# Performance work log

Measured on AMD Instinct MI355X. Metric: run time of the kernel, lower is better.

The kernel has to match this reference:

```python
import jax, jax.numpy as jnp
import numpy as np

NUM_HEADS = 12


def setup_inputs() -> dict:
    key = jax.random.key(0)
    ks = jax.random.split(key, 8)
    B, D, H, W, C = 4, 8, 14, 14, 768
    hd = C // NUM_HEADS
    return {
        "x": jax.random.normal(ks[0], (B, D, H, W, C), jnp.float32),
        "qkv_w": jax.random.normal(ks[1], (C, 3 * C), jnp.float32) * (C ** -0.5),
        "qkv_b": jax.random.normal(ks[2], (3 * C,), jnp.float32) * 0.02,
        "proj_w": jax.random.normal(ks[3], (C, C), jnp.float32) * (C ** -0.5),
        "proj_b": jax.random.normal(ks[4], (C,), jnp.float32) * 0.02,
        "rel_pos_d": jax.random.normal(ks[5], (2 * D - 1, hd), jnp.float32) * 0.02,
        "rel_pos_h": jax.random.normal(ks[6], (2 * H - 1, hd), jnp.float32) * 0.02,
        "rel_pos_w": jax.random.normal(ks[7], (2 * W - 1, hd), jnp.float32) * 0.02,
    }


def _rel_table(table, n):
    # q_size == k_size == n; relative coords in [0, 2n-2]
    idx = jnp.arange(n)[:, None] - jnp.arange(n)[None, :] + (n - 1)
    return table[idx]  # [n, n, head_dim]


def reference(x, qkv_w, qkv_b, proj_w, proj_b, rel_pos_d, rel_pos_h, rel_pos_w):
    B, D, H, W, C = x.shape
    hd = C // NUM_HEADS
    scale = hd ** -0.5
    N = D * H * W
    BH = B * NUM_HEADS

    qkv = x @ qkv_w + qkv_b  # [B,D,H,W,3C]
    qkv = qkv.reshape(B, N, 3, NUM_HEADS, hd).transpose(2, 0, 3, 1, 4).reshape(3, BH, N, hd)
    q, k, v = qkv[0], qkv[1], qkv[2]

    attn = jnp.einsum('bnc,bmc->bnm', q * scale, k)  # [BH, N, N]

    # decomposed 3D relative position bias
    Rd = _rel_table(rel_pos_d, D)  # [D,D,hd]
    Rh = _rel_table(rel_pos_h, H)  # [H,H,hd]
    Rw = _rel_table(rel_pos_w, W)  # [W,W,hd]
    r_q = q.reshape(BH, D, H, W, hd)
    rel_d = jnp.einsum('bdhwc,dkc->bdhwk', r_q, Rd)  # [BH,D,H,W,D]
    rel_h = jnp.einsum('bdhwc,hkc->bdhwk', r_q, Rh)  # [BH,D,H,W,H]
    rel_w = jnp.einsum('bdhwc,wkc->bdhwk', r_q, Rw)  # [BH,D,H,W,W]
    attn = (attn.reshape(BH, D, H, W, D, H, W)
            + rel_d[:, :, :, :, :, None, None]
            + rel_h[:, :, :, :, None, :, None]
            + rel_w[:, :, :, :, None, None, :]).reshape(BH, N, N)

    attn = jax.nn.softmax(attn, axis=-1)
    out = jnp.einsum('bnm,bmc->bnc', attn, v)  # [BH,N,hd]
    out = out.reshape(B, NUM_HEADS, D, H, W, hd).transpose(0, 2, 3, 4, 1, 5).reshape(B, D, H, W, C)
    return out @ proj_w + proj_b
```

## Files before the change

kernel.cpp:

```cpp
#include <hip/hip_runtime.h>


typedef __bf16 bf16x8 __attribute__((ext_vector_type(8)));
typedef float f32x4 __attribute__((ext_vector_type(4)));

#define MFMA16(a, b, c) __builtin_amdgcn_mfma_f32_16x16x32_bf16((a), (b), (c), 0, 0, 0)

static __device__ __forceinline__ unsigned short f2bf(float f) {
    union { float f; unsigned int u; } v; v.f = f;
    unsigned int u = v.u;
    return (unsigned short)((u + 0x7fffu + ((u >> 16) & 1u)) >> 16);
}

static __device__ __forceinline__ bf16x8 ld_bf8(const unsigned short* p) {
    return *reinterpret_cast<const bf16x8*>(p);
}

static __device__ __forceinline__ void dma16(const void* g, void* l) {
    __builtin_amdgcn_global_load_lds(
        (const __attribute__((address_space(1))) void*)g,
        (__attribute__((address_space(3))) void*)l, 16, 0, 0);
}


__global__ void k_cvt_x(const float* __restrict__ x, unsigned short* __restrict__ xbf, int n4) {
    int i = blockIdx.x * blockDim.x + threadIdx.x;
    if (i < n4) {
        float4 v = reinterpret_cast<const float4*>(x)[i];
        ushort4 o;
        o.x = f2bf(v.x); o.y = f2bf(v.y); o.z = f2bf(v.z); o.w = f2bf(v.w);
        reinterpret_cast<ushort4*>(xbf)[i] = o;
    }
}

__global__ __launch_bounds__(256) void k_transpose(const float* __restrict__ w,
                                                   unsigned short* __restrict__ wt,
                                                   int K, int N) {
    __shared__ float tile[64][65];
    int kt = blockIdx.x * 64;
    int nt = blockIdx.y * 64;
    int tid = threadIdx.x;
    int r = tid >> 2;
    int cg = tid & 3;
#pragma unroll
    for (int i = 0; i < 4; ++i) {
        int c = cg * 16 + i * 4;
        float4 v = *reinterpret_cast<const float4*>(&w[(size_t)(kt + r) * N + nt + c]);
        tile[r][c + 0] = v.x; tile[r][c + 1] = v.y; tile[r][c + 2] = v.z; tile[r][c + 3] = v.w;
    }
    __syncthreads();
#pragma unroll
    for (int i = 0; i < 4; ++i) {
        int c = cg * 16 + i * 4;
        ushort4 o;
        o.x = f2bf(tile[c + 0][r]);
        o.y = f2bf(tile[c + 1][r]);
        o.z = f2bf(tile[c + 2][r]);
        o.w = f2bf(tile[c + 3][r]);
        *reinterpret_cast<ushort4*>(&wt[(size_t)(nt + r) * K + kt + c]) = o;
    }
}

__global__ void k_tables(const float* __restrict__ rd, const float* __restrict__ rh,
                         const float* __restrict__ rw, unsigned short* __restrict__ T) {
    int i = blockIdx.x * blockDim.x + threadIdx.x;
    if (i < 80 * 64) {
        int row = i >> 6, c = i & 63;
        float v = 0.f;
        if (row < 15) v = rd[row * 64 + c];
        else if (row < 42) v = rh[(row - 15) * 64 + c];
        else if (row < 69) v = rw[(row - 42) * 64 + c];
        T[i] = f2bf(v);
    }
}

__global__ void k_fill_ind(unsigned short* __restrict__ indb) {
    int i = blockIdx.x * blockDim.x + threadIdx.x;
    if (i < 1600 * 64) {
        int key = i >> 6, c = i & 63;
        unsigned short v = 0;
        if (key < 1568) {
            int kd = key / 196;
            int r = key - kd * 196;
            int kh = r / 14;
            int kw = r - kh * 14;
            if (c == kd || c == 8 + kh || c == 22 + kw) v = 0x3F80;
        } else {
            if (c == 36) v = 0x3F80;
        }
        indb[i] = v;
    }
}

static __device__ __forceinline__ void gemm_core(const unsigned short* __restrict__ A,
                                                 const unsigned short* __restrict__ B,
                                                 int M_base, int N_base,
                                                 char* smem, f32x4 acc[4][4]) {
    const int lane = threadIdx.x & 63;
    const int wid = threadIdx.x >> 6;
    const int ww = wid & 1, wh = wid >> 1;
    const int quad = lane >> 4, l16 = lane & 15;
    const int sr = lane >> 3, sc = lane & 7;
    unsigned short* sA = (unsigned short*)smem;
    unsigned short* sB = (unsigned short*)(smem + 16384);

    for (int kt = 0; kt < 12; ++kt) {
#pragma unroll
        for (int j = 0; j < 4; ++j) {
            int loc = wid * 32 + j * 8 + sr;
            int gc = ((sc + loc) & 7) * 16;
            dma16((const char*)A + (size_t)(M_base + loc) * 1536 + kt * 128 + gc,
                  (char*)sA + (wid * 32 + j * 8) * 128);
            dma16((const char*)B + (size_t)(N_base + loc) * 1536 + kt * 128 + gc,
                  (char*)sB + (wid * 32 + j * 8) * 128);
        }
        __syncthreads();
#pragma unroll
        for (int s = 0; s < 2; ++s) {
            bf16x8 af[4], bfr[4];
#pragma unroll
            for (int i = 0; i < 4; ++i) {
                int ar = wh * 64 + i * 16 + l16;
                af[i] = ld_bf8(sA + ar * 64 + (((s * 4 + quad) - ar) & 7) * 8);
                int br = ww * 64 + i * 16 + l16;
                bfr[i] = ld_bf8(sB + br * 64 + (((s * 4 + quad) - br) & 7) * 8);
            }
#pragma unroll
            for (int i = 0; i < 4; ++i)
#pragma unroll
                for (int j2 = 0; j2 < 4; ++j2)
                    acc[i][j2] = MFMA16(af[i], bfr[j2], acc[i][j2]);
        }
        __syncthreads();
    }
}

__global__ __launch_bounds__(256, 3) void k_qkv(const unsigned short* __restrict__ xbf,
                                                const unsigned short* __restrict__ w1t,
                                                const float* __restrict__ qkv_b,
                                                unsigned short* __restrict__ qb,
                                                unsigned short* __restrict__ kb2,
                                                unsigned short* __restrict__ vb) {
    __shared__ __align__(16) char smem[32768];
    f32x4 acc[4][4] = {};
    gemm_core(xbf, w1t, blockIdx.x * 128, blockIdx.y * 128, smem, acc);

    const int lane = threadIdx.x & 63;
    const int wid = threadIdx.x >> 6;
    const int ww = wid & 1, wh = wid >> 1;
    const int quad = lane >> 4, l16 = lane & 15;
#pragma unroll
    for (int j = 0; j < 4; ++j) {
        int n = blockIdx.y * 128 + ww * 64 + j * 16 + l16;
        float bias = qkv_b[n];
        int which = n / 768;
        int rem = n - which * 768;
        int head = rem >> 6;
        int c = rem & 63;
#pragma unroll
        for (int i = 0; i < 4; ++i) {
#pragma unroll
            for (int r = 0; r < 4; ++r) {
                int m = blockIdx.x * 128 + wh * 64 + i * 16 + quad * 4 + r;
                float val = acc[i][j][r] + bias;
                int b_ = m / 1568;
                int nn = m - b_ * 1568;
                size_t idx = ((size_t)(b_ * 12 + head) * 1568 + nn) * 64 + c;
                if (which == 0)      qb[idx] = f2bf(val);
                else if (which == 1) kb2[(((size_t)(b_ * 12 + head)) * 1600 + nn) * 64 + c] = f2bf(val * 0.125f);
                else                 vb[idx] = f2bf(val);
            }
        }
    }
}

__global__ __launch_bounds__(256) void k_vt(const unsigned short* __restrict__ vb,
                                            unsigned short* __restrict__ vtb) {
    __shared__ unsigned short t[64][72];
    int bh = blockIdx.y;
    int n0 = blockIdx.x * 64;
    int tid = threadIdx.x;
    int r = tid >> 2, cg = (tid & 3) * 16;
    int n = n0 + r;
    if (n > 1567) n = 1567;
    const unsigned short* src = vb + ((size_t)bh * 1568 + n) * 64 + cg;
    *reinterpret_cast<uint4*>(&t[r][cg]) = *reinterpret_cast<const uint4*>(src);
    *reinterpret_cast<uint4*>(&t[r][cg + 8]) = *reinterpret_cast<const uint4*>(src + 8);
    __syncthreads();
    int c = tid >> 2, ng = (tid & 3) * 16;
    if (n0 + ng < 1568) {
        unsigned short buf[16];
#pragma unroll
        for (int i = 0; i < 16; ++i) buf[i] = t[ng + i][c];
        unsigned short* dst = vtb + ((size_t)bh * 64 + c) * 1600 + n0 + ng;
        *reinterpret_cast<uint4*>(dst) = *reinterpret_cast<uint4*>(&buf[0]);
        *reinterpret_cast<uint4*>(dst + 8) = *reinterpret_cast<uint4*>(&buf[8]);
    }
}

__global__ __launch_bounds__(256, 3) void k_attn(const unsigned short* __restrict__ qb,
                                                 const unsigned short* __restrict__ kb2,
                                                 const unsigned short* __restrict__ indb,
                                                 const unsigned short* __restrict__ vtb,
                                                 const unsigned short* __restrict__ Tbf,
                                                 unsigned short* __restrict__ obf) {
    __shared__ __align__(16) char smem[43008];
    unsigned short* sK = (unsigned short*)smem;
    unsigned short* sI = (unsigned short*)(smem + 8192);
    unsigned short* sV = (unsigned short*)(smem + 16384);
    const int lane = threadIdx.x & 63;
    const int wid = threadIdx.x >> 6;
    const int quad = lane >> 4;
    const int l16 = lane & 15;
    const int sr = lane >> 3;
    const int sc = lane & 7;
    const int bh = blockIdx.x;
    const int qt = blockIdx.y;

    unsigned short* pw = (unsigned short*)(smem + 24576 + wid * 4608);
    unsigned short* tR = (unsigned short*)(smem + wid * 5120);
    unsigned short* tB = (unsigned short*)(smem + 20480 + wid * 4608);

    bf16x8 a_q0[2], a_q1[2], a_b0[2], a_b1[2];
#pragma unroll
    for (int mt = 0; mt < 2; ++mt) {
        int qrow = qt * 128 + wid * 32 + mt * 16 + l16;
        if (qrow > 1567) qrow = 1567;
        const unsigned short* qp = qb + ((size_t)bh * 1568 + qrow) * 64 + quad * 8;
        a_q0[mt] = ld_bf8(qp);
        a_q1[mt] = ld_bf8(qp + 32);
    }
#pragma unroll
    for (int mt = 0; mt < 2; ++mt) {
#pragma unroll
        for (int ng = 0; ng < 5; ++ng) {
            const unsigned short* tp = Tbf + (size_t)(ng * 16 + l16) * 64 + quad * 8;
            f32x4 t = {};
            t = MFMA16(a_q0[mt], ld_bf8(tp), t);
            t = MFMA16(a_q1[mt], ld_bf8(tp + 32), t);
#pragma unroll
            for (int r = 0; r < 4; ++r)
                tR[(mt * 16 + quad * 4 + r) * 80 + ng * 16 + l16] = f2bf(t[r]);
        }
    }
#pragma unroll
    for (int mt = 0; mt < 2; ++mt) {
        int gq = qt * 128 + wid * 32 + mt * 16 + l16;
        if (gq > 1567) gq = 1567;
        int qd = gq / 196;
        int rm = gq - qd * 196;
        int qh = rm / 14;
        int qw = rm - qh * 14;
        const unsigned short* qr = tR + (mt * 16 + l16) * 80;
        unsigned short* qxr = tB + (mt * 16 + l16) * 72;
#pragma unroll
        for (int t = 0; t < 16; ++t) {
            int dd = quad * 16 + t;
            unsigned short v = 0;
            if (dd < 8)        v = qr[qd - dd + 7];
            else if (dd < 22)  v = qr[15 + qh - (dd - 8) + 13];
            else if (dd < 36)  v = qr[42 + qw - (dd - 22) + 13];
            else if (dd == 36) v = 0xC6EA;
            qxr[dd] = v;
        }
    }
#pragma unroll
    for (int mt = 0; mt < 2; ++mt) {
        const unsigned short* qx = tB + (mt * 16 + l16) * 72;
        a_b0[mt] = ld_bf8(qx + quad * 8);
        a_b1[mt] = ld_bf8(qx + 32 + quad * 8);
    }
    __syncthreads();

    float l_i[2][4] = {};
    f32x4 Oacc[2][4] = {};

    const char* kbh_b = (const char*)(kb2 + (size_t)bh * 1600 * 64);
    const char* ind_b = (const char*)indb;
    const char* vbh_b = (const char*)(vtb + (size_t)bh * 64 * 1600);

    for (int kt = 0; kt < 25; ++kt) {
        const int kb0 = kt * 64;
#pragma unroll
        for (int j = 0; j < 2; ++j) {
            int loc = wid * 16 + j * 8 + sr;
            int gc = ((sc + loc) & 7) * 16;
            char* dK = (char*)sK + (wid * 16 + j * 8) * 128;
            char* dI = (char*)sI + (wid * 16 + j * 8) * 128;
            char* dV = (char*)sV + (wid * 16 + j * 8) * 128;
            dma16(kbh_b + (size_t)(kb0 + loc) * 128 + gc, dK);
            dma16(ind_b + (size_t)(kb0 + loc) * 128 + gc, dI);
            dma16(vbh_b + (size_t)loc * 3200 + (size_t)kb0 * 2 + gc, dV);
        }
        __syncthreads();

        float p[2][4][4];
        float rs[2][4] = {};
#pragma unroll
        for (int kg = 0; kg < 4; ++kg) {
            int key = kg * 16 + l16;
            const unsigned short* kr = sK + key * 64;
            const unsigned short* ir = sI + key * 64;
            bf16x8 bk0 = ld_bf8(kr + ((quad - key) & 7) * 8);
            bf16x8 bk1 = ld_bf8(kr + ((quad + 4 - key) & 7) * 8);
            bf16x8 bi0 = ld_bf8(ir + ((quad - key) & 7) * 8);
            bf16x8 bi1 = ld_bf8(ir + ((quad + 4 - key) & 7) * 8);
#pragma unroll
            for (int mt = 0; mt < 2; ++mt) {
                f32x4 t = {};
                t = MFMA16(a_q0[mt], bk0, t);
                t = MFMA16(a_q1[mt], bk1, t);
                t = MFMA16(a_b0[mt], bi0, t);
                t = MFMA16(a_b1[mt], bi1, t);
#pragma unroll
                for (int r = 0; r < 4; ++r) {
                    float pv = __expf(t[r]);
                    p[mt][kg][r] = pv;
                    rs[mt][r] += pv;
                }
            }
        }
#pragma unroll
        for (int mt = 0; mt < 2; ++mt)
#pragma unroll
            for (int r = 0; r < 4; ++r) {
                float v = rs[mt][r];
                v += __shfl_xor(v, 1);
                v += __shfl_xor(v, 2);
                v += __shfl_xor(v, 4);
                v += __shfl_xor(v, 8);
                l_i[mt][r] += v;
            }
#pragma unroll
        for (int mt = 0; mt < 2; ++mt)
#pragma unroll
            for (int kg = 0; kg < 4; ++kg)
#pragma unroll
                for (int r = 0; r < 4; ++r)
                    pw[(mt * 16 + quad * 4 + r) * 72 + kg * 16 + l16] = f2bf(p[mt][kg][r]);
        bf16x8 ap0[2], ap1[2];
#pragma unroll
        for (int mt = 0; mt < 2; ++mt) {
            const unsigned short* pr = pw + (mt * 16 + l16) * 72;
            ap0[mt] = ld_bf8(pr + quad * 8);
            ap1[mt] = ld_bf8(pr + 32 + quad * 8);
        }
#pragma unroll
        for (int cg = 0; cg < 4; ++cg) {
            int dim = cg * 16 + l16;
            const unsigned short* vr = sV + dim * 64;
            bf16x8 v0 = ld_bf8(vr + ((quad - dim) & 7) * 8);
            bf16x8 v1 = ld_bf8(vr + ((quad + 4 - dim) & 7) * 8);
#pragma unroll
            for (int mt = 0; mt < 2; ++mt) {
                Oacc[mt][cg] = MFMA16(ap0[mt], v0, Oacc[mt][cg]);
                Oacc[mt][cg] = MFMA16(ap1[mt], v1, Oacc[mt][cg]);
            }
        }
        __syncthreads();
    }

    int b_ = bh / 12;
    int head = bh - b_ * 12;
    unsigned short* ob = obf + (size_t)b_ * 1568 * 768 + head * 64;
#pragma unroll
    for (int mt = 0; mt < 2; ++mt)
#pragma unroll
        for (int r = 0; r < 4; ++r) {
            int gq = qt * 128 + wid * 32 + mt * 16 + quad * 4 + r;
            if (gq < 1568) {
                float inv = 1.0f / l_i[mt][r];
#pragma unroll
                for (int cg = 0; cg < 4; ++cg)
                    ob[(size_t)gq * 768 + cg * 16 + l16] = f2bf(Oacc[mt][cg][r] * inv);
            }
        }
}

__global__ __launch_bounds__(256, 3) void k_proj(const unsigned short* __restrict__ obf,
                                                 const unsigned short* __restrict__ w2t,
                                                 const float* __restrict__ proj_b,
                                                 float* __restrict__ out) {
    __shared__ __align__(16) char smem[32768];
    f32x4 acc[4][4] = {};
    gemm_core(obf, w2t, blockIdx.x * 128, blockIdx.y * 128, smem, acc);

    const int lane = threadIdx.x & 63;
    const int wid = threadIdx.x >> 6;
    const int ww = wid & 1, wh = wid >> 1;
    const int quad = lane >> 4, l16 = lane & 15;
#pragma unroll
    for (int j = 0; j < 4; ++j) {
        int n = blockIdx.y * 128 + ww * 64 + j * 16 + l16;
        float bias = proj_b[n];
#pragma unroll
        for (int i = 0; i < 4; ++i) {
#pragma unroll
            for (int r = 0; r < 4; ++r) {
                int m = blockIdx.x * 128 + wh * 64 + i * 16 + quad * 4 + r;
                out[(size_t)m * 768 + n] = acc[i][j][r] + bias;
            }
        }
    }
}

extern "C" void kernel_launch(void* const* d_in, const int* in_sizes, int n_in,
                              void* d_out, int out_size, void* d_ws, size_t ws_size,
                              hipStream_t stream) {
    const float* x      = (const float*)d_in[0];
    const float* qkv_w  = (const float*)d_in[1];
    const float* qkv_b  = (const float*)d_in[2];
    const float* proj_w = (const float*)d_in[3];
    const float* proj_b = (const float*)d_in[4];
    const float* rd     = (const float*)d_in[5];
    const float* rh     = (const float*)d_in[6];
    const float* rw     = (const float*)d_in[7];
    float* out = (float*)d_out;

    char* ws = (char*)d_ws;
    size_t off = 0;
    auto alloc = [&](size_t bytes) {
        char* p = ws + off;
        off += (bytes + 255) & ~(size_t)255;
        return p;
    };
    unsigned short* xbf  = (unsigned short*)alloc((size_t)6272 * 768 * 2);
    unsigned short* w1t  = (unsigned short*)alloc((size_t)2304 * 768 * 2);
    unsigned short* w2t  = (unsigned short*)alloc((size_t)768 * 768 * 2);
    unsigned short* Tbf  = (unsigned short*)alloc((size_t)80 * 64 * 2);
    unsigned short* qb   = (unsigned short*)alloc((size_t)48 * 1568 * 64 * 2);
    unsigned short* kb2  = (unsigned short*)alloc((size_t)48 * 1600 * 64 * 2);
    unsigned short* vtb  = (unsigned short*)alloc((size_t)48 * 64 * 1600 * 2);
    unsigned short* indb = (unsigned short*)alloc((size_t)1600 * 64 * 2);
    unsigned short* obf  = xbf;
    unsigned short* vb   = (unsigned short*)d_out;

    hipLaunchKernelGGL(k_cvt_x, dim3(4704), dim3(256), 0, stream, x, xbf, 1204224);
    hipLaunchKernelGGL(k_transpose, dim3(12, 36), dim3(256), 0, stream, qkv_w, w1t, 768, 2304);
    hipLaunchKernelGGL(k_transpose, dim3(12, 12), dim3(256), 0, stream, proj_w, w2t, 768, 768);
    hipLaunchKernelGGL(k_tables, dim3(20), dim3(256), 0, stream, rd, rh, rw, Tbf);
    hipLaunchKernelGGL(k_fill_ind, dim3(400), dim3(256), 0, stream, indb);
    hipLaunchKernelGGL(k_qkv, dim3(49, 18), dim3(256), 0, stream, xbf, w1t, qkv_b, qb, kb2, vb);
    hipLaunchKernelGGL(k_vt, dim3(25, 48), dim3(256), 0, stream, vb, vtb);
    hipLaunchKernelGGL(k_attn, dim3(48, 13), dim3(256), 0, stream, qb, kb2, indb, vtb, Tbf, obf);
    hipLaunchKernelGGL(k_proj, dim3(49, 6), dim3(256), 0, stream, obf, w2t, proj_b, out);
}
```

Baseline: 269.6 us.

## Double-buffer K/I/V tiles, use exp2 with prescaled log2e, defer row-sum reduction

```diff
diff --git a/kernel.cpp b/kernel.cpp
--- a/kernel.cpp
+++ b/kernel.cpp
@@ -5,6 +5,12 @@
 typedef float f32x4 __attribute__((ext_vector_type(4)));
 
 #define MFMA16(a, b, c) __builtin_amdgcn_mfma_f32_16x16x32_bf16((a), (b), (c), 0, 0, 0)
+
+#if __has_builtin(__builtin_amdgcn_exp2f)
+#define EXP2(x) __builtin_amdgcn_exp2f(x)
+#else
+#define EXP2(x) exp2f(x)
+#endif
 
 static __device__ __forceinline__ unsigned short f2bf(float f) {
     union { float f; unsigned int u; } v; v.f = f;
@@ -70,7 +76,7 @@
         if (row < 15) v = rd[row * 64 + c];
         else if (row < 42) v = rh[(row - 15) * 64 + c];
         else if (row < 69) v = rw[(row - 42) * 64 + c];
-        T[i] = f2bf(v);
+        T[i] = f2bf(v * 1.44269504f);
     }
 }
 
@@ -167,7 +173,7 @@
                 int nn = m - b_ * 1568;
                 size_t idx = ((size_t)(b_ * 12 + head) * 1568 + nn) * 64 + c;
                 if (which == 0)      qb[idx] = f2bf(val);
-                else if (which == 1) kb2[(((size_t)(b_ * 12 + head)) * 1600 + nn) * 64 + c] = f2bf(val * 0.125f);
+                else if (which == 1) kb2[(((size_t)(b_ * 12 + head)) * 1600 + nn) * 64 + c] = f2bf(val * 0.18033688f);
                 else                 vb[idx] = f2bf(val);
             }
         }
@@ -198,16 +204,13 @@
     }
 }
 
-__global__ __launch_bounds__(256, 3) void k_attn(const unsigned short* __restrict__ qb,
+__global__ __launch_bounds__(256, 2) void k_attn(const unsigned short* __restrict__ qb,
                                                  const unsigned short* __restrict__ kb2,
                                                  const unsigned short* __restrict__ indb,
                                                  const unsigned short* __restrict__ vtb,
                                                  const unsigned short* __restrict__ Tbf,
                                                  unsigned short* __restrict__ obf) {
-    __shared__ __align__(16) char smem[43008];
-    unsigned short* sK = (unsigned short*)smem;
-    unsigned short* sI = (unsigned short*)(smem + 8192);
-    unsigned short* sV = (unsigned short*)(smem + 16384);
+    __shared__ __align__(16) char smem[58368];
     const int lane = threadIdx.x & 63;
     const int wid = threadIdx.x >> 6;
     const int quad = lane >> 4;
@@ -217,9 +220,9 @@
     const int bh = blockIdx.x;
     const int qt = blockIdx.y;
 
-    unsigned short* pw = (unsigned short*)(smem + 24576 + wid * 4608);
+    unsigned short* pw = (unsigned short*)(smem + 49152 + wid * 2304);
     unsigned short* tR = (unsigned short*)(smem + wid * 5120);
-    unsigned short* tB = (unsigned short*)(smem + 20480 + wid * 4608);
+    unsigned short* tB = (unsigned short*)(smem + 24576 + wid * 4608);
 
     bf16x8 a_q0[2], a_q1[2], a_b0[2], a_b1[2];
 #pragma unroll
@@ -272,30 +275,37 @@
     }
     __syncthreads();
 
-    float l_i[2][4] = {};
-    f32x4 Oacc[2][4] = {};
-
     const char* kbh_b = (const char*)(kb2 + (size_t)bh * 1600 * 64);
     const char* ind_b = (const char*)indb;
     const char* vbh_b = (const char*)(vtb + (size_t)bh * 64 * 1600);
 
-    for (int kt = 0; kt < 25; ++kt) {
-        const int kb0 = kt * 64;
+    auto stage = [&](char* sbase, int kb0) {
 #pragma unroll
         for (int j = 0; j < 2; ++j) {
             int loc = wid * 16 + j * 8 + sr;
             int gc = ((sc + loc) & 7) * 16;
-            char* dK = (char*)sK + (wid * 16 + j * 8) * 128;
-            char* dI = (char*)sI + (wid * 16 + j * 8) * 128;
-            char* dV = (char*)sV + (wid * 16 + j * 8) * 128;
-            dma16(kbh_b + (size_t)(kb0 + loc) * 128 + gc, dK);
-            dma16(ind_b + (size_t)(kb0 + loc) * 128 + gc, dI);
-            dma16(vbh_b + (size_t)loc * 3200 + (size_t)kb0 * 2 + gc, dV);
-        }
-        __syncthreads();
+            char* d = sbase + (wid * 16 + j * 8) * 128;
+            dma16(kbh_b + (size_t)(kb0 + loc) * 128 + gc, d);
+            dma16(ind_b + (size_t)(kb0 + loc) * 128 + gc, d + 8192);
+            dma16(vbh_b + (size_t)loc * 3200 + (size_t)kb0 * 2 + gc, d + 16384);
+        }
+    };
+
+    float l_p[2][4] = {};
+    f32x4 Oacc[2][4] = {};
+
+    stage(smem, 0);
+    __syncthreads();
+
+    for (int kt = 0; kt < 25; ++kt) {
+        char* cur = smem + (kt & 1) * 24576;
+        if (kt < 24) stage(smem + ((kt + 1) & 1) * 24576, (kt + 1) * 64);
+
+        const unsigned short* sK = (const unsigned short*)cur;
+        const unsigned short* sI = (const unsigned short*)(cur + 8192);
+        const unsigned short* sV = (const unsigned short*)(cur + 16384);
 
         float p[2][4][4];
-        float rs[2][4] = {};
 #pragma unroll
         for (int kg = 0; kg < 4; ++kg) {
             int key = kg * 16 + l16;
@@ -314,47 +324,39 @@
                 t = MFMA16(a_b1[mt], bi1, t);
 #pragma unroll
                 for (int r = 0; r < 4; ++r) {
-                    float pv = __expf(t[r]);
-                    p[mt][kg][r] = pv;
-                    rs[mt][r] += pv;
+                    union { float f; unsigned int u; } c;
+                    c.f = EXP2(t[r]);
+                    c.u &= 0xFFFF0000u;
+                    p[mt][kg][r] = c.f;
+                    l_p[mt][r] += c.f;
                 }
             }
         }
-#pragma unroll
-        for (int mt = 0; mt < 2; ++mt)
-#pragma unroll
-            for (int r = 0; r < 4; ++r) {
-                float v = rs[mt][r];
-                v += __shfl_xor(v, 1);
-                v += __shfl_xor(v, 2);
-                v += __shfl_xor(v, 4);
-                v += __shfl_xor(v, 8);
-                l_i[mt][r] += v;
-            }
-#pragma unroll
-        for (int mt = 0; mt < 2; ++mt)
-#pragma unroll
-            for (int kg = 0; kg < 4; ++kg)
-#pragma unroll
-                for (int r = 0; r < 4; ++r)
-                    pw[(mt * 16 + quad * 4 + r) * 72 + kg * 16 + l16] = f2bf(p[mt][kg][r]);
-        bf16x8 ap0[2], ap1[2];
-#pragma unroll
-        for (int mt = 0; mt < 2; ++mt) {
-            const unsigned short* pr = pw + (mt * 16 + l16) * 72;
-            ap0[mt] = ld_bf8(pr + quad * 8);
-            ap1[mt] = ld_bf8(pr + 32 + quad * 8);
-        }
+        bf16x8 v0[4], v1[4];
 #pragma unroll
         for (int cg = 0; cg < 4; ++cg) {
             int dim = cg * 16 + l16;
             const unsigned short* vr = sV + dim * 64;
-            bf16x8 v0 = ld_bf8(vr + ((quad - dim) & 7) * 8);
-            bf16x8 v1 = ld_bf8(vr + ((quad + 4 - dim) & 7) * 8);
-#pragma unroll
-            for (int mt = 0; mt < 2; ++mt) {
-                Oacc[mt][cg] = MFMA16(ap0[mt], v0, Oacc[mt][cg]);
-                Oacc[mt][cg] = MFMA16(ap1[mt], v1, Oacc[mt][cg]);
+            v0[cg] = ld_bf8(vr + ((quad - dim) & 7) * 8);
+            v1[cg] = ld_bf8(vr + ((quad + 4 - dim) & 7) * 8);
+        }
+#pragma unroll
+        for (int mt = 0; mt < 2; ++mt) {
+#pragma unroll
+            for (int kg = 0; kg < 4; ++kg)
+#pragma unroll
+                for (int r = 0; r < 4; ++r) {
+                    union { float f; unsigned int u; } c;
+                    c.f = p[mt][kg][r];
+                    pw[(quad * 4 + r) * 72 + kg * 16 + l16] = (unsigned short)(c.u >> 16);
+                }
+            const unsigned short* pr = pw + l16 * 72;
+            bf16x8 ap0 = ld_bf8(pr + quad * 8);
+            bf16x8 ap1 = ld_bf8(pr + 32 + quad * 8);
+#pragma unroll
+            for (int cg = 0; cg < 4; ++cg) {
+                Oacc[mt][cg] = MFMA16(ap0, v0[cg], Oacc[mt][cg]);
+                Oacc[mt][cg] = MFMA16(ap1, v1[cg], Oacc[mt][cg]);
             }
         }
         __syncthreads();
@@ -367,9 +369,14 @@
     for (int mt = 0; mt < 2; ++mt)
 #pragma unroll
         for (int r = 0; r < 4; ++r) {
+            float v = l_p[mt][r];
+            v += __shfl_xor(v, 1);
+            v += __shfl_xor(v, 2);
+            v += __shfl_xor(v, 4);
+            v += __shfl_xor(v, 8);
             int gq = qt * 128 + wid * 32 + mt * 16 + quad * 4 + r;
             if (gq < 1568) {
-                float inv = 1.0f / l_i[mt][r];
+                float inv = 1.0f / v;
 #pragma unroll
                 for (int cg = 0; cg < 4; ++cg)
                     ob[(size_t)gq * 768 + cg * 16 + l16] = f2bf(Oacc[mt][cg][r] * inv);
```

Result: faster. 245.0 us (-9.1%).
